# Optimization experiments

Measured on AMD Instinct MI355X. Metric: run time of the kernel, lower is better.

The kernel has to match this reference:

```python
import jax, jax.numpy as jnp
import numpy as np

K = 1024          # num_embeddings (static for segment_sum)
D = 256           # embedding_dim
B, H, W = 32, 64, 64
DECAY = 0.99
EPS = 1e-05
BETA = 0.25


def setup_inputs() -> dict:
    key = jax.random.key(0)
    k1, k2 = jax.random.split(key)
    z = jax.random.normal(k1, (B, D, H, W), dtype=jnp.float32)
    embedding = jax.random.normal(k2, (K, D), dtype=jnp.float32)
    ema_cluster_size = jnp.zeros((K,), dtype=jnp.float32)
    ema_embedding = embedding.copy()
    return {"z": z, "embedding": embedding,
            "ema_cluster_size": ema_cluster_size,
            "ema_embedding": ema_embedding}


def reference(z, embedding, ema_cluster_size, ema_embedding):
    b, d, h, w = z.shape
    # (B, D, H, W) -> (B*H*W, D)
    z_flat = jnp.transpose(z, (0, 2, 3, 1)).reshape(-1, d)
    # squared L2 distances to each code: ||z||^2 - 2 z.E^T + ||E||^2  -> (N, K)
    dist = (jnp.sum(z_flat * z_flat, axis=1, keepdims=True)
            - 2.0 * (z_flat @ embedding.T)
            + jnp.sum(embedding * embedding, axis=1))
    encoding_indices = jnp.argmin(dist, axis=1)                 # (N,)
    # one-hot @ embedding == gather
    quantized = embedding[encoding_indices]                     # (N, D)
    quantized = jnp.transpose(quantized.reshape(b, h, w, d), (0, 3, 1, 2))
    # EMA buffer updates (encodings.sum(0) and encodings.T @ z_flat as segment sums)
    counts = jax.ops.segment_sum(jnp.ones_like(encoding_indices, dtype=z.dtype),
                                 encoding_indices, num_segments=K)
    dw = jax.ops.segment_sum(z_flat, encoding_indices, num_segments=K)
    new_cluster_size = DECAY * ema_cluster_size + (1.0 - DECAY) * counts
    new_ema_embedding = DECAY * ema_embedding + (1.0 - DECAY) * dw
    # straight-through estimator
    quantized_ste = z + jax.lax.stop_gradient(quantized - z)
    commitment_loss = BETA * jnp.mean(jnp.square(z - jax.lax.stop_gradient(quantized_ste)))
    return (quantized_ste, commitment_loss, encoding_indices,
            new_cluster_size, new_ema_embedding)
```

## Files before the change

### kernel.cpp

```cpp
#include <hip/hip_runtime.h>

#define KC 1024
#define DD 256
#define NP 131072
#define HWSZ 4096
#define TOTZ 33554432

#define OUT_Q    0
#define OUT_LOSS 33554432
#define OUT_IDX  33554433
#define OUT_CS   33685505
#define OUT_EMA  33686529

#define WS_IDX    0
#define WS_COUNTS 131072
#define WS_RCNT   132096
#define WS_LOSSP  132352
#define WS_ENORM  132608
#define WS_RLIST  133632
#define WS_EAUG   264704
#define WS_ZAUG   657920
#define WS_NEED_FLOATS (WS_ZAUG + 33554432)

#define MARGIN 0.0625f
#define RTILE 16

typedef __attribute__((ext_vector_type(8))) short bf16x8;
typedef __attribute__((ext_vector_type(4))) float f32x4;

__device__ inline unsigned short f2bf_rne(float x) {
    unsigned u = __float_as_uint(x);
    unsigned r = u + 0x7FFFu + ((u >> 16) & 1u);
    return (unsigned short)(r >> 16);
}
__device__ inline float bf2f(unsigned short h) {
    return __uint_as_float(((unsigned)h) << 16);
}
__device__ inline void gl_lds16(const void* g, void* l) {
    __builtin_amdgcn_global_load_lds(
        (const __attribute__((address_space(1))) unsigned int*)g,
        (__attribute__((address_space(3))) unsigned int*)l, 16, 0, 0);
}
__device__ inline unsigned long long packkey(float d, int c) {
    unsigned u = __float_as_uint(d);
    u = (u & 0x80000000u) ? ~u : (u | 0x80000000u);
    return (((unsigned long long)u) << 32) | (unsigned)c;
}

__global__ __launch_bounds__(256) void enorm_kernel(const float* __restrict__ emb,
                                                    float* __restrict__ enorm) {
    const int k = blockIdx.x;
    float v = emb[k * DD + threadIdx.x];
    v *= v;
    #pragma unroll
    for (int off = 32; off > 0; off >>= 1) v += __shfl_down(v, off);
    __shared__ float red[4];
    if ((threadIdx.x & 63) == 0) red[threadIdx.x >> 6] = v;
    __syncthreads();
    if (threadIdx.x == 0) enorm[k] = (red[0] + red[1]) + (red[2] + red[3]);
}

__global__ __launch_bounds__(256) void convert_z_kernel(
    const float* __restrict__ z, unsigned short* __restrict__ zaug)
{
    const int blk = blockIdx.x;
    const int pt = blk >> 2, kslot = blk & 3;
    const int kbase0 = kslot * 64;
    unsigned short* outH = zaug + (size_t)(pt * 8 + kslot) * 8192;
    unsigned short* outM = zaug + (size_t)(pt * 8 + 4 + kslot) * 8192;
    #pragma unroll
    for (int i = 0; i < 4; ++i) {
        const int f = i * 256 + threadIdx.x;
        const int kc = f >> 9, mt = (f >> 6) & 7, lane = f & 63;
        const int q = lane >> 4, col = lane & 15;
        const int p = pt * 128 + mt * 16 + col;
        const int b = p >> 12, hw = p & 4095;
        const int k0 = kbase0 + kc * 32 + q * 8;
        const float* src = z + (size_t)b * 1048576 + (size_t)k0 * 4096 + hw;
        unsigned short vh[8], vm[8];
        #pragma unroll
        for (int j = 0; j < 8; ++j) {
            const float x = src[j * 4096];
            const unsigned short h = f2bf_rne(x);
            vh[j] = h;
            vm[j] = f2bf_rne(x - bf2f(h));
        }
        *(uint4*)(outH + (size_t)f * 8) = *(uint4*)vh;
        *(uint4*)(outM + (size_t)f * 8) = *(uint4*)vm;
    }
}

__global__ __launch_bounds__(256) void convert_emb_kernel(
    const float* __restrict__ emb, unsigned short* __restrict__ eaug)
{
    const int blk = blockIdx.x;
    const int cc = blk / 12, ks = blk % 12;
    const int mode = (ks >= 8);
    unsigned short* outp = eaug + (size_t)blk * 8192;
    #pragma unroll
    for (int i = 0; i < 4; ++i) {
        const int f = i * 256 + threadIdx.x;
        const int kc = f >> 9, nt = (f >> 6) & 7, lane = f & 63;
        const int q = lane >> 4, col = lane & 15;
        const int n = cc * 128 + nt * 16 + col;
        const int k0 = ((ks * 64) & 255) + kc * 32 + q * 8;
        const float* src = emb + (size_t)n * 256 + k0;
        unsigned short v[8];
        #pragma unroll
        for (int j = 0; j < 8; ++j) {
            const float x = src[j];
            const unsigned short h = f2bf_rne(x);
            v[j] = mode ? f2bf_rne(x - bf2f(h)) : h;
        }
        *(uint4*)(outp + (size_t)f * 8) = *(uint4*)v;
    }
}

__global__ __launch_bounds__(512) void gemm_argmin_kernel(
    const unsigned short* __restrict__ zaug, const unsigned short* __restrict__ eaug,
    const float* __restrict__ enorm, int* __restrict__ idx_out,
    float* __restrict__ idx_out_f, float* __restrict__ counts,
    int* __restrict__ rcnt, int* __restrict__ rlist)
{
    __shared__ float smem[32768];
    unsigned short* aS = (unsigned short*)smem;
    const int t = threadIdx.x, w = t >> 6, lane = t & 63;
    const int mh = w & 1, nq = w >> 1;
    const int col = lane & 15;
    const int pt = blockIdx.x;

    float rb[16], rs[16]; int ri[16];
    #pragma unroll
    for (int s = 0; s < 16; ++s) { rb[s] = 3.4e38f; rs[s] = 3.4e38f; ri[s] = 0; }

    const unsigned short* zb = zaug + (size_t)pt * 65536;

    #pragma unroll
    for (int i = 0; i < 8; ++i) {
        const int off = i * 4096 + w * 512 + lane * 8;
        gl_lds16(zb + off, aS + off);
    }
    __syncthreads();
    #pragma unroll
    for (int i = 8; i < 16; ++i) {
        const int off = i * 4096 + w * 512 + lane * 8;
        gl_lds16(zb + off, aS + off);
    }

    #pragma unroll 1
    for (int g = 0; g < 4; ++g) {
        const int ccg = g * 2 + (nq >> 1);
        const int nbase = ccg * 128 + (nq & 1) * 64;
        const unsigned short* eb = eaug + (size_t)ccg * (12 * 8192)
                                 + (nq & 1) * 2048 + (size_t)lane * 8;
        f32x4 acc[4][4];
        #pragma unroll
        for (int mi = 0; mi < 4; ++mi)
            #pragma unroll
            for (int ni = 0; ni < 4; ++ni) acc[mi][ni] = (f32x4){0.f, 0.f, 0.f, 0.f};
        float en[4];
        #pragma unroll
        for (int ni = 0; ni < 4; ++ni) en[ni] = enorm[nbase + ni * 16 + col];

        bf16x8 bcur[2][4], bnxt[2][4];
        #pragma unroll
        for (int kc = 0; kc < 2; ++kc)
            #pragma unroll
            for (int ni = 0; ni < 4; ++ni)
                bcur[kc][ni] = *(const bf16x8*)(eb + kc * 4096 + ni * 512);

        #pragma unroll 1
        for (int j = 0; j < 12; ++j) {
            if (g == 0 && j == 8) __syncthreads();
            const int slab = (j < 8) ? (j & 3) : (4 + (j & 3));
            if (j < 11) {
                const int jn = j + 1;
                const int ksn = (jn < 4) ? jn : ((jn < 8) ? jn + 4 : jn - 4);
                const unsigned short* ebk = eb + (size_t)ksn * 8192;
                #pragma unroll
                for (int kc = 0; kc < 2; ++kc)
                    #pragma unroll
                    for (int ni = 0; ni < 4; ++ni)
                        bnxt[kc][ni] = *(const bf16x8*)(ebk + kc * 4096 + ni * 512);
            }
            #pragma unroll
            for (int kc = 0; kc < 2; ++kc) {
                bf16x8 af[4];
                #pragma unroll
                for (int mi = 0; mi < 4; ++mi)
                    af[mi] = *(const bf16x8*)(aS + slab * 8192 + kc * 4096
                                              + (mh * 4 + mi) * 512 + lane * 8);
                #pragma unroll
                for (int mi = 0; mi < 4; ++mi)
                    #pragma unroll
                    for (int ni = 0; ni < 4; ++ni)
                        acc[mi][ni] = __builtin_amdgcn_mfma_f32_16x16x32_bf16(
                            af[mi], bcur[kc][ni], acc[mi][ni], 0, 0, 0);
            }
            #pragma unroll
            for (int kc = 0; kc < 2; ++kc)
                #pragma unroll
                for (int ni = 0; ni < 4; ++ni)
                    bcur[kc][ni] = bnxt[kc][ni];
        }
        #pragma unroll
        for (int mi = 0; mi < 4; ++mi) {
            #pragma unroll
            for (int r = 0; r < 4; ++r) {
                const int s = mi * 4 + r;
                float v0 = fmaf(-2.f, acc[mi][0][r], en[0]);
                float v1 = fmaf(-2.f, acc[mi][1][r], en[1]);
                float v2 = fmaf(-2.f, acc[mi][2][r], en[2]);
                float v3 = fmaf(-2.f, acc[mi][3][r], en[3]);
                const int nb = nbase + col;
                float b01 = fminf(v0, v1), x01 = fmaxf(v0, v1);
                int   i01 = (v1 < v0) ? nb + 16 : nb;
                float b23 = fminf(v2, v3), x23 = fmaxf(v2, v3);
                int   i23 = (v3 < v2) ? nb + 48 : nb + 32;
                float b = fminf(b01, b23);
                int   ib = (b23 < b01) ? i23 : i01;
                float s2 = fminf(fmaxf(b01, b23), fminf(x01, x23));
                if (b < rb[s]) { rs[s] = fminf(rb[s], s2); rb[s] = b; ri[s] = ib; }
                else           { rs[s] = fminf(rs[s], b); }
            }
        }
    }

    float* rbS = smem;
    float* rsS = smem + 4096;
    int*   riS = (int*)(smem + 8192);
    #pragma unroll 1
    for (int ph = 0; ph < 2; ++ph) {
        __syncthreads();
        if (mh == ph) {
            #pragma unroll
            for (int s = 0; s < 16; ++s) {
                rbS[nq * 1024 + s * 64 + lane] = rb[s];
                rsS[nq * 1024 + s * 64 + lane] = rs[s];
                riS[nq * 1024 + s * 64 + lane] = ri[s];
            }
        }
        __syncthreads();
        if (t < 64) {
            const int r = t;
            const int mi = r >> 4, q = (r >> 2) & 3, rr = r & 3;
            const int s = mi * 4 + rr;
            float B = 3.4e38f, S = 3.4e38f; int I = 0;
            #pragma unroll
            for (int wv = 0; wv < 4; ++wv) {
                const int base = wv * 1024 + s * 64 + q * 16;
                #pragma unroll
                for (int ln = 0; ln < 16; ++ln) {
                    const float b = rbS[base + ln];
                    const float s2 = rsS[base + ln];
                    const int   i = riS[base + ln];
                    if (b < B) { S = fminf(B, s2); B = b; I = i; }
                    else       { S = fminf(S, b); }
                }
            }
            const int p = pt * 128 + ph * 64 + r;
            idx_out[p] = I;
            idx_out_f[p] = (float)I;
            atomicAdd(&counts[I], 1.0f);
            if (S - B < MARGIN) {
                const int pos = atomicAdd(rcnt, 1);
                rlist[pos] = p;
            }
        }
    }
}

__global__ __launch_bounds__(256) void rescue_kernel(
    const float* __restrict__ z, const float* __restrict__ emb,
    const float* __restrict__ enorm, const int* __restrict__ rcnt,
    const int* __restrict__ rlist, int* __restrict__ idx_out,
    float* __restrict__ idx_out_f, float* __restrict__ counts)
{
    __shared__ float zl[RTILE][DD];
    __shared__ unsigned long long lkey[RTILE];
    const int n = *rcnt;
    if (n <= 0) return;
    const int ntiles = (n + RTILE - 1) / RTILE;
    const int t = threadIdx.x;
    const int slot = t & 15, drow = t >> 4;
    #pragma unroll 1
    for (int tile = blockIdx.x; tile < ntiles; tile += gridDim.x) {
        const int base = tile * RTILE;
        {
            const int ridx = min(base + slot, n - 1);
            const int p = rlist[ridx];
            const int b = p >> 12, hw = p & 4095;
            const float* zp = z + (size_t)b * 1048576 + hw;
            #pragma unroll
            for (int j = 0; j < 16; ++j)
                zl[slot][drow * 16 + j] = zp[(size_t)(drow * 16 + j) * 4096];
        }
        if (t < RTILE) lkey[t] = ~0ull;
        __syncthreads();
        float dot[RTILE][4];
        #pragma unroll
        for (int p = 0; p < RTILE; ++p)
            #pragma unroll
            for (int ci = 0; ci < 4; ++ci) dot[p][ci] = 0.f;
        #pragma unroll 1
        for (int d4 = 0; d4 < 64; ++d4) {
            float4 ev[4];
            #pragma unroll
            for (int ci = 0; ci < 4; ++ci)
                ev[ci] = *(const float4*)(emb + (size_t)(ci * 256 + t) * 256 + d4 * 4);
            #pragma unroll
            for (int p = 0; p < RTILE; ++p) {
                const float4 zv = *(const float4*)(&zl[p][d4 * 4]);
                #pragma unroll
                for (int ci = 0; ci < 4; ++ci) {
                    dot[p][ci] = fmaf(zv.x, ev[ci].x, dot[p][ci]);
                    dot[p][ci] = fmaf(zv.y, ev[ci].y, dot[p][ci]);
                    dot[p][ci] = fmaf(zv.z, ev[ci].z, dot[p][ci]);
                    dot[p][ci] = fmaf(zv.w, ev[ci].w, dot[p][ci]);
                }
            }
        }
        float en[4];
        #pragma unroll
        for (int ci = 0; ci < 4; ++ci) en[ci] = enorm[ci * 256 + t];
        #pragma unroll
        for (int p = 0; p < RTILE; ++p) {
            unsigned long long k = packkey(fmaf(-2.f, dot[p][0], en[0]), t);
            #pragma unroll
            for (int ci = 1; ci < 4; ++ci) {
                const unsigned long long k2 =
                    packkey(fmaf(-2.f, dot[p][ci], en[ci]), ci * 256 + t);
                k = (k2 < k) ? k2 : k;
            }
            atomicMin(&lkey[p], k);
        }
        __syncthreads();
        if (t < RTILE && base + t < n) {
            const int p = rlist[base + t];
            const int fc = (int)(lkey[t] & 0xFFFFFFFFull);
            const int old = idx_out[p];
            if (fc != old) {
                atomicAdd(&counts[old], -1.0f);
                atomicAdd(&counts[fc], 1.0f);
                idx_out[p] = fc;
                idx_out_f[p] = (float)fc;
            }
        }
        __syncthreads();
    }
}

__global__ __launch_bounds__(512) void dwq_kernel(
    const float* __restrict__ z, const float* __restrict__ emb,
    const int* __restrict__ idx, const float* __restrict__ ema_emb,
    float* __restrict__ out_q, float* __restrict__ out_ema,
    float* __restrict__ lossp)
{
    __shared__ float kdw[KC];
    __shared__ float ecol[KC];
    __shared__ float red[8];
    const int d = blockIdx.x;
    const int t = threadIdx.x;
    #pragma unroll
    for (int k = t; k < KC; k += 512) { kdw[k] = 0.f; ecol[k] = emb[(size_t)k * 256 + d]; }
    __syncthreads();
    float ls = 0.f;
    #pragma unroll 1
    for (int it = 0; it < 64; ++it) {
        const int e = it * 512 + t;
        const int b = e >> 10, hwi = (e & 1023) << 2;
        const size_t zoff = (size_t)b * 1048576 + (size_t)d * 4096 + hwi;
        const float4 zv = *(const float4*)(z + zoff);
        const int4 iv = *(const int4*)(idx + b * 4096 + hwi);
        const float q0 = ecol[iv.x], q1 = ecol[iv.y], q2 = ecol[iv.z], q3 = ecol[iv.w];
        float4 qv; qv.x = q0; qv.y = q1; qv.z = q2; qv.w = q3;
        *(float4*)(out_q + zoff) = qv;
        atomicAdd(&kdw[iv.x], zv.x);
        atomicAdd(&kdw[iv.y], zv.y);
        atomicAdd(&kdw[iv.z], zv.z);
        atomicAdd(&kdw[iv.w], zv.w);
        const float d0 = zv.x - q0, d1 = zv.y - q1, d2 = zv.z - q2, d3 = zv.w - q3;
        ls += (d0 * d0 + d1 * d1) + (d2 * d2 + d3 * d3);
    }
    __syncthreads();
    #pragma unroll
    for (int k = t; k < KC; k += 512)
        out_ema[(size_t)k * 256 + d] = 0.99f * ema_emb[(size_t)k * 256 + d] + 0.01f * kdw[k];
    #pragma unroll
    for (int off = 32; off > 0; off >>= 1) ls += __shfl_down(ls, off);
    if ((t & 63) == 0) red[t >> 6] = ls;
    __syncthreads();
    if (t == 0) {
        float s = 0.f;
        #pragma unroll
        for (int i = 0; i < 8; ++i) s += red[i];
        lossp[blockIdx.x] = s;
    }
}

__global__ __launch_bounds__(256) void finalize_kernel(
    const float* __restrict__ ema_cs, const float* __restrict__ counts,
    const float* __restrict__ lossp, float* __restrict__ out)
{
    const int i = blockIdx.x * 256 + threadIdx.x;
    out[OUT_CS + i] = 0.99f * ema_cs[i] + 0.01f * counts[i];
    if (blockIdx.x == 0) {
        float s = lossp[threadIdx.x];
        #pragma unroll
        for (int off = 32; off > 0; off >>= 1) s += __shfl_down(s, off);
        __shared__ float red[4];
        if ((threadIdx.x & 63) == 0) red[threadIdx.x >> 6] = s;
        __syncthreads();
        if (threadIdx.x == 0)
            out[OUT_LOSS] = 0.25f * ((red[0] + red[1]) + (red[2] + red[3])) / 33554432.0f;
    }
}

__global__ __launch_bounds__(256) void dist_argmin_kernel(
    const float* __restrict__ z, const float* __restrict__ emb,
    const float* __restrict__ enorm, int* __restrict__ idx_out,
    float* __restrict__ idx_out_f, float* __restrict__ counts)
{
    __shared__ float smem[4096];
    float* As = smem;
    float* Bs = smem + 1024;
    const int tid = threadIdx.x;
    const int tx = tid & 15, ty = tid >> 4;
    const int p0 = blockIdx.x * 128;
    const int b = p0 >> 12, hw0 = p0 & 4095;
    const float* zb = z + (size_t)b * (DD * HWSZ) + hw0;
    const int arow = (tid & 31) * 4, akd = tid >> 5;
    const int bcode = tid >> 1, bj = (tid & 1) * 4;
    float best[8]; int bidx[8];
    #pragma unroll
    for (int i = 0; i < 8; i++) { best[i] = 3.4e38f; bidx[i] = 0; }
    #pragma unroll 1
    for (int cc = 0; cc < 8; ++cc) {
        const int c0 = cc * 128;
        float acc[8][8];
        #pragma unroll
        for (int i = 0; i < 8; i++)
            #pragma unroll
            for (int j = 0; j < 8; j++) acc[i][j] = 0.0f;
        #pragma unroll 1
        for (int dk = 0; dk < 32; ++dk) {
            const int kk0 = dk * 8;
            const float4 av = *(const float4*)(zb + (kk0 + akd) * HWSZ + arow);
            const float4 bv = *(const float4*)(emb + (c0 + bcode) * DD + kk0 + bj);
            __syncthreads();
            *(float4*)(As + akd * 128 + arow) = av;
            Bs[(bj + 0) * 128 + bcode] = bv.x;
            Bs[(bj + 1) * 128 + bcode] = bv.y;
            Bs[(bj + 2) * 128 + bcode] = bv.z;
            Bs[(bj + 3) * 128 + bcode] = bv.w;
            __syncthreads();
            #pragma unroll
            for (int kk = 0; kk < 8; ++kk) {
                const float4 a0 = *(const float4*)(As + kk * 128 + ty * 8);
                const float4 a1 = *(const float4*)(As + kk * 128 + ty * 8 + 4);
                const float4 b0 = *(const float4*)(Bs + kk * 128 + tx * 8);
                const float4 b1 = *(const float4*)(Bs + kk * 128 + tx * 8 + 4);
                const float a[8] = {a0.x,a0.y,a0.z,a0.w,a1.x,a1.y,a1.z,a1.w};
                const float bb[8] = {b0.x,b0.y,b0.z,b0.w,b1.x,b1.y,b1.z,b1.w};
                #pragma unroll
                for (int i = 0; i < 8; i++)
                    #pragma unroll
                    for (int j = 0; j < 8; j++)
                        acc[i][j] = fmaf(a[i], bb[j], acc[i][j]);
            }
        }
        const float4 en0 = *(const float4*)(enorm + c0 + tx * 8);
        const float4 en1 = *(const float4*)(enorm + c0 + tx * 8 + 4);
        const float en[8] = {en0.x,en0.y,en0.z,en0.w,en1.x,en1.y,en1.z,en1.w};
        #pragma unroll
        for (int j = 0; j < 8; j++) {
            const int c = c0 + tx * 8 + j;
            #pragma unroll
            for (int i = 0; i < 8; i++) {
                const float dist = fmaf(-2.0f, acc[i][j], en[j]);
                if (dist < best[i]) { best[i] = dist; bidx[i] = c; }
            }
        }
    }
    __syncthreads();
    float* rmin = smem;
    int* ridx = (int*)(smem + 2048);
    #pragma unroll
    for (int i = 0; i < 8; i++) {
        const int r = ty * 8 + i;
        rmin[r * 16 + tx] = best[i];
        ridx[r * 16 + tx] = bidx[i];
    }
    __syncthreads();
    if (tid < 128) {
        const int r = tid;
        float m = rmin[r * 16]; int mi = ridx[r * 16];
        #pragma unroll
        for (int tt = 1; tt < 16; tt++) {
            const float v = rmin[r * 16 + tt];
            const int vi = ridx[r * 16 + tt];
            if (v < m || (v == m && vi < mi)) { m = v; mi = vi; }
        }
        const int p = p0 + r;
        idx_out[p] = mi;
        idx_out_f[p] = (float)mi;
        atomicAdd(&counts[mi], 1.0f);
    }
}

extern "C" void kernel_launch(void* const* d_in, const int* in_sizes, int n_in,
                              void* d_out, int out_size, void* d_ws, size_t ws_size,
                              hipStream_t stream) {
    const float* z       = (const float*)d_in[0];
    const float* emb     = (const float*)d_in[1];
    const float* ema_cs  = (const float*)d_in[2];
    const float* ema_emb = (const float*)d_in[3];
    float* out = (float*)d_out;
    float* ws  = (float*)d_ws;

    int*   ws_idx    = (int*)(ws + WS_IDX);
    float* ws_counts = ws + WS_COUNTS;
    int*   ws_rcnt   = (int*)(ws + WS_RCNT);
    float* ws_lossp  = ws + WS_LOSSP;
    float* ws_enorm  = ws + WS_ENORM;
    int*   ws_rlist  = (int*)(ws + WS_RLIST);
    unsigned short* ws_eaug = (unsigned short*)(ws + WS_EAUG);
    unsigned short* ws_zaug = (unsigned short*)(ws + WS_ZAUG);

    hipMemsetAsync(ws_counts, 0, 1025 * sizeof(float), stream);
    hipLaunchKernelGGL(enorm_kernel, dim3(KC), dim3(256), 0, stream, emb, ws_enorm);

    if (ws_size >= (size_t)WS_NEED_FLOATS * sizeof(float)) {
        hipLaunchKernelGGL(convert_z_kernel, dim3(4096), dim3(256), 0, stream, z, ws_zaug);
        hipLaunchKernelGGL(convert_emb_kernel, dim3(96), dim3(256), 0, stream, emb, ws_eaug);
        hipLaunchKernelGGL(gemm_argmin_kernel, dim3(1024), dim3(512), 0, stream,
                           ws_zaug, ws_eaug, ws_enorm, ws_idx, out + OUT_IDX,
                           ws_counts, ws_rcnt, ws_rlist);
        hipLaunchKernelGGL(rescue_kernel, dim3(512), dim3(256), 0, stream,
                           z, emb, ws_enorm, ws_rcnt, ws_rlist,
                           ws_idx, out + OUT_IDX, ws_counts);
    } else {
        hipLaunchKernelGGL(dist_argmin_kernel, dim3(NP / 128), dim3(256), 0, stream,
                           z, emb, ws_enorm, ws_idx, out + OUT_IDX, ws_counts);
    }

    hipLaunchKernelGGL(dwq_kernel, dim3(DD), dim3(512), 0, stream,
                       z, emb, ws_idx, ema_emb, out, out + OUT_EMA, ws_lossp);
    hipLaunchKernelGGL(finalize_kernel, dim3(4), dim3(256), 0, stream,
                       ema_cs, ws_counts, ws_lossp, out);
}
```

Baseline: 800.8 us.

## Fuse z bf16 split conversion into GEMM-argmin and shrink tile to 64 rows

Removes the separate convert_z kernel and its 128 MB workspace round trip. Each GEMM block now loads fp32 z directly and writes the hi/lo bf16 split into LDS itself. The block shrinks from 512 to 256 threads covering 64 points, with half the LDS and two blocks per CU. The K-loop is also fully unrolled and s_setprio is wrapped around the MFMA bursts. The cost is that the E fragments are now read from global memory twice as often (once per 64 points instead of per 128), and the strided fp32 z loads sit on the GEMM's critical path.

```diff
diff --git a/kernel.cpp b/kernel.cpp
--- a/kernel.cpp
+++ b/kernel.cpp
@@ -19,8 +19,7 @@
 #define WS_ENORM  132608
 #define WS_RLIST  133632
 #define WS_EAUG   264704
-#define WS_ZAUG   657920
-#define WS_NEED_FLOATS (WS_ZAUG + 33554432)
+#define WS_NEED_FLOATS (WS_EAUG + 393216)
 
 #define MARGIN 0.0625f
 #define RTILE 16
@@ -35,11 +34,6 @@
 }
 __device__ inline float bf2f(unsigned short h) {
     return __uint_as_float(((unsigned)h) << 16);
-}
-__device__ inline void gl_lds16(const void* g, void* l) {
-    __builtin_amdgcn_global_load_lds(
-        (const __attribute__((address_space(1))) unsigned int*)g,
-        (__attribute__((address_space(3))) unsigned int*)l, 16, 0, 0);
 }
 __device__ inline unsigned long long packkey(float d, int c) {
     unsigned u = __float_as_uint(d);
@@ -58,36 +52,6 @@
     if ((threadIdx.x & 63) == 0) red[threadIdx.x >> 6] = v;
     __syncthreads();
     if (threadIdx.x == 0) enorm[k] = (red[0] + red[1]) + (red[2] + red[3]);
-}
-
-__global__ __launch_bounds__(256) void convert_z_kernel(
-    const float* __restrict__ z, unsigned short* __restrict__ zaug)
-{
-    const int blk = blockIdx.x;
-    const int pt = blk >> 2, kslot = blk & 3;
-    const int kbase0 = kslot * 64;
-    unsigned short* outH = zaug + (size_t)(pt * 8 + kslot) * 8192;
-    unsigned short* outM = zaug + (size_t)(pt * 8 + 4 + kslot) * 8192;
-    #pragma unroll
-    for (int i = 0; i < 4; ++i) {
-        const int f = i * 256 + threadIdx.x;
-        const int kc = f >> 9, mt = (f >> 6) & 7, lane = f & 63;
-        const int q = lane >> 4, col = lane & 15;
-        const int p = pt * 128 + mt * 16 + col;
-        const int b = p >> 12, hw = p & 4095;
-        const int k0 = kbase0 + kc * 32 + q * 8;
-        const float* src = z + (size_t)b * 1048576 + (size_t)k0 * 4096 + hw;
-        unsigned short vh[8], vm[8];
-        #pragma unroll
-        for (int j = 0; j < 8; ++j) {
-            const float x = src[j * 4096];
-            const unsigned short h = f2bf_rne(x);
-            vh[j] = h;
-            vm[j] = f2bf_rne(x - bf2f(h));
-        }
-        *(uint4*)(outH + (size_t)f * 8) = *(uint4*)vh;
-        *(uint4*)(outM + (size_t)f * 8) = *(uint4*)vm;
-    }
 }
 
 __global__ __launch_bounds__(256) void convert_emb_kernel(
@@ -116,36 +80,48 @@
     }
 }
 
-__global__ __launch_bounds__(512) void gemm_argmin_kernel(
-    const unsigned short* __restrict__ zaug, const unsigned short* __restrict__ eaug,
+__global__ __launch_bounds__(256, 2) void gemm_argmin_kernel(
+    const float* __restrict__ z, const unsigned short* __restrict__ eaug,
     const float* __restrict__ enorm, int* __restrict__ idx_out,
     float* __restrict__ idx_out_f, float* __restrict__ counts,
     int* __restrict__ rcnt, int* __restrict__ rlist)
 {
-    __shared__ float smem[32768];
+    __shared__ float smem[16384];
     unsigned short* aS = (unsigned short*)smem;
     const int t = threadIdx.x, w = t >> 6, lane = t & 63;
-    const int mh = w & 1, nq = w >> 1;
+    const int nq = w;
     const int col = lane & 15;
     const int pt = blockIdx.x;
 
+    #pragma unroll
+    for (int jj0 = 0; jj0 < 8; ++jj0) {
+        const int jj = jj0 * 256 + t;
+        const int kslot = jj >> 9;
+        const int r = jj & 511;
+        const int kc = r >> 8, mt = (r >> 6) & 3, lf = r & 63;
+        const int q = lf >> 4, cl = lf & 15;
+        const int p = pt * 64 + mt * 16 + cl;
+        const int b = p >> 12, hw = p & 4095;
+        const int k0 = kslot * 64 + kc * 32 + q * 8;
+        const float* src = z + (size_t)b * 1048576 + (size_t)k0 * 4096 + hw;
+        unsigned short vh[8], vm[8];
+        #pragma unroll
+        for (int i = 0; i < 8; ++i) {
+            const float x = src[i * 4096];
+            const unsigned short h = f2bf_rne(x);
+            vh[i] = h;
+            vm[i] = f2bf_rne(x - bf2f(h));
+        }
+        const int off = kc * 2048 + mt * 512 + lf * 8;
+        *(uint4*)(aS + kslot * 4096 + off) = *(uint4*)vh;
+        *(uint4*)(aS + (4 + kslot) * 4096 + off) = *(uint4*)vm;
+    }
+
     float rb[16], rs[16]; int ri[16];
     #pragma unroll
     for (int s = 0; s < 16; ++s) { rb[s] = 3.4e38f; rs[s] = 3.4e38f; ri[s] = 0; }
 
-    const unsigned short* zb = zaug + (size_t)pt * 65536;
-
-    #pragma unroll
-    for (int i = 0; i < 8; ++i) {
-        const int off = i * 4096 + w * 512 + lane * 8;
-        gl_lds16(zb + off, aS + off);
-    }
-    __syncthreads();
-    #pragma unroll
-    for (int i = 8; i < 16; ++i) {
-        const int off = i * 4096 + w * 512 + lane * 8;
-        gl_lds16(zb + off, aS + off);
-    }
+    __syncthreads();
 
     #pragma unroll 1
     for (int g = 0; g < 4; ++g) {
@@ -169,9 +145,8 @@
             for (int ni = 0; ni < 4; ++ni)
                 bcur[kc][ni] = *(const bf16x8*)(eb + kc * 4096 + ni * 512);
 
-        #pragma unroll 1
+        #pragma unroll
         for (int j = 0; j < 12; ++j) {
-            if (g == 0 && j == 8) __syncthreads();
             const int slab = (j < 8) ? (j & 3) : (4 + (j & 3));
             if (j < 11) {
                 const int jn = j + 1;
@@ -188,20 +163,24 @@
                 bf16x8 af[4];
                 #pragma unroll
                 for (int mi = 0; mi < 4; ++mi)
-                    af[mi] = *(const bf16x8*)(aS + slab * 8192 + kc * 4096
-                                              + (mh * 4 + mi) * 512 + lane * 8);
+                    af[mi] = *(const bf16x8*)(aS + slab * 4096 + kc * 2048
+                                              + mi * 512 + lane * 8);
+                __builtin_amdgcn_s_setprio(1);
                 #pragma unroll
                 for (int mi = 0; mi < 4; ++mi)
                     #pragma unroll
                     for (int ni = 0; ni < 4; ++ni)
                         acc[mi][ni] = __builtin_amdgcn_mfma_f32_16x16x32_bf16(
                             af[mi], bcur[kc][ni], acc[mi][ni], 0, 0, 0);
-            }
-            #pragma unroll
-            for (int kc = 0; kc < 2; ++kc)
+                __builtin_amdgcn_s_setprio(0);
+            }
+            if (j < 11) {
                 #pragma unroll
-                for (int ni = 0; ni < 4; ++ni)
-                    bcur[kc][ni] = bnxt[kc][ni];
+                for (int kc = 0; kc < 2; ++kc)
+                    #pragma unroll
+                    for (int ni = 0; ni < 4; ++ni)
+                        bcur[kc][ni] = bnxt[kc][ni];
+            }
         }
         #pragma unroll
         for (int mi = 0; mi < 4; ++mi) {
@@ -226,46 +205,41 @@
         }
     }
 
+    __syncthreads();
     float* rbS = smem;
     float* rsS = smem + 4096;
     int*   riS = (int*)(smem + 8192);
-    #pragma unroll 1
-    for (int ph = 0; ph < 2; ++ph) {
-        __syncthreads();
-        if (mh == ph) {
-            #pragma unroll
-            for (int s = 0; s < 16; ++s) {
-                rbS[nq * 1024 + s * 64 + lane] = rb[s];
-                rsS[nq * 1024 + s * 64 + lane] = rs[s];
-                riS[nq * 1024 + s * 64 + lane] = ri[s];
-            }
-        }
-        __syncthreads();
-        if (t < 64) {
-            const int r = t;
-            const int mi = r >> 4, q = (r >> 2) & 3, rr = r & 3;
-            const int s = mi * 4 + rr;
-            float B = 3.4e38f, S = 3.4e38f; int I = 0;
-            #pragma unroll
-            for (int wv = 0; wv < 4; ++wv) {
-                const int base = wv * 1024 + s * 64 + q * 16;
-                #pragma unroll
-                for (int ln = 0; ln < 16; ++ln) {
-                    const float b = rbS[base + ln];
-                    const float s2 = rsS[base + ln];
-                    const int   i = riS[base + ln];
-                    if (b < B) { S = fminf(B, s2); B = b; I = i; }
-                    else       { S = fminf(S, b); }
-                }
-            }
-            const int p = pt * 128 + ph * 64 + r;
-            idx_out[p] = I;
-            idx_out_f[p] = (float)I;
-            atomicAdd(&counts[I], 1.0f);
-            if (S - B < MARGIN) {
-                const int pos = atomicAdd(rcnt, 1);
-                rlist[pos] = p;
-            }
+    #pragma unroll
+    for (int s = 0; s < 16; ++s) {
+        rbS[w * 1024 + s * 64 + lane] = rb[s];
+        rsS[w * 1024 + s * 64 + lane] = rs[s];
+        riS[w * 1024 + s * 64 + lane] = ri[s];
+    }
+    __syncthreads();
+    if (t < 64) {
+        const int r = t;
+        const int mi = r >> 4, q = (r >> 2) & 3, rr = r & 3;
+        const int s = mi * 4 + rr;
+        float B = 3.4e38f, S = 3.4e38f; int I = 0;
+        #pragma unroll
+        for (int wv = 0; wv < 4; ++wv) {
+            const int base = wv * 1024 + s * 64 + q * 16;
+            #pragma unroll
+            for (int ln = 0; ln < 16; ++ln) {
+                const float b = rbS[base + ln];
+                const float s2 = rsS[base + ln];
+                const int   i = riS[base + ln];
+                if (b < B) { S = fminf(B, s2); B = b; I = i; }
+                else       { S = fminf(S, b); }
+            }
+        }
+        const int p = pt * 64 + r;
+        idx_out[p] = I;
+        idx_out_f[p] = (float)I;
+        atomicAdd(&counts[I], 1.0f);
+        if (S - B < MARGIN) {
+            const int pos = atomicAdd(rcnt, 1);
+            rlist[pos] = p;
         }
     }
 }
@@ -525,16 +499,14 @@
     float* ws_enorm  = ws + WS_ENORM;
     int*   ws_rlist  = (int*)(ws + WS_RLIST);
     unsigned short* ws_eaug = (unsigned short*)(ws + WS_EAUG);
-    unsigned short* ws_zaug = (unsigned short*)(ws + WS_ZAUG);
 
     hipMemsetAsync(ws_counts, 0, 1025 * sizeof(float), stream);
     hipLaunchKernelGGL(enorm_kernel, dim3(KC), dim3(256), 0, stream, emb, ws_enorm);
 
     if (ws_size >= (size_t)WS_NEED_FLOATS * sizeof(float)) {
-        hipLaunchKernelGGL(convert_z_kernel, dim3(4096), dim3(256), 0, stream, z, ws_zaug);
         hipLaunchKernelGGL(convert_emb_kernel, dim3(96), dim3(256), 0, stream, emb, ws_eaug);
-        hipLaunchKernelGGL(gemm_argmin_kernel, dim3(1024), dim3(512), 0, stream,
-                           ws_zaug, ws_eaug, ws_enorm, ws_idx, out + OUT_IDX,
+        hipLaunchKernelGGL(gemm_argmin_kernel, dim3(2048), dim3(256), 0, stream,
+                           z, ws_eaug, ws_enorm, ws_idx, out + OUT_IDX,
                            ws_counts, ws_rcnt, ws_rlist);
         hipLaunchKernelGGL(rescue_kernel, dim3(512), dim3(256), 0, stream,
                            z, emb, ws_enorm, ws_rcnt, ws_rlist,
```

Result: slower. 1.159 ms (+44.8%).
